# Performance work log

Measured on AMD Instinct MI355X. Metric: run time of the kernel, lower is better.

Reference implementation:

```python
import jax, jax.numpy as jnp
import numpy as np

HID = 1024
HEADS = 16
HEAD_DIM = HID // HEADS
MAX_P = 64
TAB = 2 * MAX_P + 1
B, L = 8, 512


def setup_inputs() -> dict:
    key = jax.random.key(0)
    ks = jax.random.split(key, 16)
    def lin(k, fan_in, fan_out):
        lim = 1.0 / np.sqrt(fan_in)
        kw, kb = jax.random.split(k)
        W = jax.random.uniform(kw, (fan_out, fan_in), jnp.float32, -lim, lim)
        b = jax.random.uniform(kb, (fan_out,), jnp.float32, -lim, lim)
        return W, b
    Wq, bq = lin(ks[0], HID, HID)
    Wk, bk = lin(ks[1], HID, HID)
    Wv, bv = lin(ks[2], HID, HID)
    Wo, bo = lin(ks[3], HID, HID)
    # xavier_uniform for relative-position tables
    xlim = float(np.sqrt(6.0 / (TAB + HEAD_DIM)))
    table_k = jax.random.uniform(ks[4], (TAB, HEAD_DIM), jnp.float32, -xlim, xlim)
    table_v = jax.random.uniform(ks[5], (TAB, HEAD_DIM), jnp.float32, -xlim, xlim)
    return {
        "query": jax.random.normal(ks[6], (B, L, HID), jnp.float32),
        "key": jax.random.normal(ks[7], (B, L, HID), jnp.float32),
        "value": jax.random.normal(ks[8], (B, L, HID), jnp.float32),
        "final_mat": jax.random.randint(ks[9], (B, L, L), 0, TAB, jnp.int64 if jax.config.jax_enable_x64 else jnp.int32),
        "Wq": Wq, "bq": bq, "Wk": Wk, "bk": bk,
        "Wv": Wv, "bv": bv, "Wo": Wo, "bo": bo,
        "table_k": table_k, "table_v": table_v,
    }


def reference(query, key, value, final_mat, Wq, bq, Wk, bk, Wv, bv, Wo, bo, table_k, table_v):
    Bt, Lq, D = query.shape
    H, hd = HEADS, HEAD_DIM
    q = query @ Wq.T + bq          # [B,Lq,D]
    k = key @ Wk.T + bk            # [B,Lk,D]
    v = value @ Wv.T + bv          # [B,Lv,D]
    q4 = q.reshape(Bt, Lq, H, hd)
    k4 = k.reshape(Bt, -1, H, hd)
    v4 = v.reshape(Bt, -1, H, hd)
    # content-content scores
    attn1 = jnp.einsum('bqhd,bkhd->bhqk', q4, k4)
    # content-position scores via gathered relative-key embeddings [B,Lq,Lk,hd]
    rk = table_k[final_mat]
    attn2 = jnp.einsum('bqhd,bqkd->bhqk', q4, rk)
    scale = jnp.asarray(np.sqrt(hd), q.dtype)
    attn = jax.nn.softmax((attn1 + attn2) / scale, axis=-1)  # [B,H,Lq,Lk]
    # dropout p=0 (eval)
    w1 = jnp.einsum('bhqk,bkhd->bqhd', attn, v4)
    rv = table_v[final_mat]                                   # [B,Lq,Lk,hd]
    w2 = jnp.einsum('bhqk,bqkd->bqhd', attn, rv)
    x = (w1 + w2).reshape(Bt, Lq, D)
    return x @ Wo.T + bo
```

## Files before the change

kernel.cpp:

```cpp
#include <hip/hip_runtime.h>

#define HID 1024
#define HEADS 16
#define HD 64
#define TAB 129
#define QSTR 136
#define BATCH 8
#define SEQ 512

typedef unsigned int uint;
typedef unsigned short ushort;
typedef unsigned char uchar;
typedef __attribute__((ext_vector_type(4))) float f32x4;
typedef __attribute__((ext_vector_type(8))) __bf16 bf16x8;

__device__ __forceinline__ ushort f2b(float x) {
    uint b = __float_as_uint(x);
    uint r = (b + 0x7fffu + ((b >> 16) & 1u)) >> 16;
    return (ushort)r;
}
__device__ __forceinline__ uint pk(float lo, float hi) {
    return (uint)f2b(lo) | ((uint)f2b(hi) << 16);
}
__device__ __forceinline__ float b2f(ushort u) {
    return __uint_as_float(((uint)u) << 16);
}
union U16x8 { uint u[4]; bf16x8 v; ushort s[8]; uint4 q; };
__device__ __forceinline__ bf16x8 pack8(float a0, float a1, float a2, float a3,
                                        float a4, float a5, float a6, float a7) {
    U16x8 r;
    r.u[0] = pk(a0, a1); r.u[1] = pk(a2, a3);
    r.u[2] = pk(a4, a5); r.u[3] = pk(a6, a7);
    return r.v;
}

#define GL16(gp, lp) __builtin_amdgcn_global_load_lds( \
    (const __attribute__((address_space(1))) void*)(gp), \
    (__attribute__((address_space(3))) void*)(lp), 16, 0, 0)

#define LDS_BARRIER() do { \
        asm volatile("s_waitcnt lgkmcnt(0)" ::: "memory"); \
        __builtin_amdgcn_s_barrier(); \
    } while (0)

struct ConvArgs { const float* src[7]; ushort* dst[7]; };

__global__ __launch_bounds__(256) void convert_bf16(ConvArgs ca) {
    int bid = blockIdx.x;
    int ti, lb;
    if (bid < 6144) { ti = bid >> 11; lb = bid & 2047; }
    else { int r = bid - 6144; ti = 3 + (r >> 9); lb = r & 511; }
    const float* s = ca.src[ti] + (size_t)lb * 2048 + (threadIdx.x << 3);
    ushort*      d = ca.dst[ti] + (size_t)lb * 2048 + (threadIdx.x << 3);
    float4 a = *(const float4*)s;
    float4 c = *(const float4*)(s + 4);
    uint4 u;
    u.x = pk(a.x, a.y); u.y = pk(a.z, a.w);
    u.z = pk(c.x, c.y); u.w = pk(c.z, c.w);
    *(uint4*)d = u;
}

struct GemmArgs {
    const ushort* A[3];
    const ushort* W[3];
    const float*  bias[3];
    ushort*       Cb[3];
};

__global__ __launch_bounds__(256) void gemm_qkv(GemmArgs ga) {
    const int N = HID, K = HID;
    __shared__ ushort As[2][128 * 32];
    __shared__ ushort Bs[2][128 * 32];
    const int tid = threadIdx.x;
    const int bid = blockIdx.x;
    const int swz = (bid & 7) * 96 + (bid >> 3);
    const int z   = swz >> 8;
    const int rem = swz & 255;
    const int m0  = (rem >> 3) * 128;
    const int n0  = (rem & 7) * 128;
    const ushort* A = ga.A[z];
    const ushort* W = ga.W[z];

    const int w  = tid >> 6;
    const int l  = tid & 63;
    const int lr = l & 15;
    const int lg = l >> 4;
    const int wm = w >> 1;
    const int wn = w & 1;

    const int sr = tid >> 2;
    const int sc = tid & 3;
    const int g  = sc ^ ((sr >> 1) & 3);
    const ushort* Ag0 = A + (size_t)(m0 + sr)      * K + g * 8;
    const ushort* Ag1 = A + (size_t)(m0 + sr + 64) * K + g * 8;
    const ushort* Wg0 = W + (size_t)(n0 + sr)      * K + g * 8;
    const ushort* Wg1 = W + (size_t)(n0 + sr + 64) * K + g * 8;

    f32x4 acc[4][4];
#pragma unroll
    for (int mt = 0; mt < 4; ++mt)
#pragma unroll
        for (int nt = 0; nt < 4; ++nt) acc[mt][nt] = (f32x4){0.f, 0.f, 0.f, 0.f};

#define STAGE(buf, k0) do { \
        GL16(Ag0 + (k0), &As[buf][w * 512]); \
        GL16(Ag1 + (k0), &As[buf][2048 + w * 512]); \
        GL16(Wg0 + (k0), &Bs[buf][w * 512]); \
        GL16(Wg1 + (k0), &Bs[buf][2048 + w * 512]); \
    } while (0)

    const int swl = (lr >> 1) & 3;
#define COMPUTE(buf) do { \
        bf16x8 af[4], bf[4]; \
        _Pragma("unroll") \
        for (int mt = 0; mt < 4; ++mt) \
            af[mt] = *(const bf16x8*)&As[buf][(wm * 64 + mt * 16 + lr) * 32 + (lg ^ swl) * 8]; \
        _Pragma("unroll") \
        for (int nt = 0; nt < 4; ++nt) \
            bf[nt] = *(const bf16x8*)&Bs[buf][(wn * 64 + nt * 16 + lr) * 32 + (lg ^ swl) * 8]; \
        _Pragma("unroll") \
        for (int mt = 0; mt < 4; ++mt) \
            _Pragma("unroll") \
            for (int nt = 0; nt < 4; ++nt) \
                acc[mt][nt] = __builtin_amdgcn_mfma_f32_16x16x32_bf16(af[mt], bf[nt], acc[mt][nt], 0, 0, 0); \
    } while (0)

    STAGE(0, 0);
    __syncthreads();
    const int nk = K / 32;
    for (int t = 0; t < nk - 1; ++t) {
        STAGE((t + 1) & 1, (size_t)(t + 1) * 32);
        COMPUTE(t & 1);
        __syncthreads();
    }
    COMPUTE((nk - 1) & 1);

    const float* bias = ga.bias[z];
    float bv[4];
#pragma unroll
    for (int nt = 0; nt < 4; ++nt) bv[nt] = bias[n0 + wn * 64 + nt * 16 + lr];
    ushort* Cb = ga.Cb[z];
#pragma unroll
    for (int mt = 0; mt < 4; ++mt)
#pragma unroll
        for (int r4 = 0; r4 < 4; ++r4) {
            size_t m = m0 + wm * 64 + mt * 16 + lg * 4 + r4;
            ushort* crow = Cb + m * N + n0 + wn * 64 + lr;
#pragma unroll
            for (int nt = 0; nt < 4; ++nt)
                crow[nt * 16] = f2b(acc[mt][nt][r4] + bv[nt]);
        }
#undef STAGE
#undef COMPUTE
}

__global__ __launch_bounds__(256) void gemm_wo(const ushort* __restrict__ A,
                                               const ushort* __restrict__ W,
                                               const float* __restrict__ bias,
                                               float* __restrict__ Cf) {
    const int N = HID, K = HID;
    __shared__ ushort As[2][128 * 32];
    __shared__ ushort Bs[2][64 * 32];
    const int tid = threadIdx.x;
    const int bid = blockIdx.x;
    const int swz = (bid & 7) * 64 + (bid >> 3);
    const int m0 = (swz >> 4) * 128;
    const int n0 = (swz & 15) * 64;

    const int w  = tid >> 6;
    const int l  = tid & 63;
    const int lr = l & 15;
    const int lg = l >> 4;
    const int wm = w >> 1;
    const int wn = w & 1;

    const int sr = tid >> 2;
    const int sc = tid & 3;
    const int g  = sc ^ ((sr >> 1) & 3);
    const ushort* Ag0 = A + (size_t)(m0 + sr)      * K + g * 8;
    const ushort* Ag1 = A + (size_t)(m0 + sr + 64) * K + g * 8;
    const ushort* Wg0 = W + (size_t)(n0 + sr)      * K + g * 8;

    f32x4 acc[4][2];
#pragma unroll
    for (int mt = 0; mt < 4; ++mt)
#pragma unroll
        for (int nt = 0; nt < 2; ++nt) acc[mt][nt] = (f32x4){0.f, 0.f, 0.f, 0.f};

#define STAGE(buf, k0) do { \
        GL16(Ag0 + (k0), &As[buf][w * 512]); \
        GL16(Ag1 + (k0), &As[buf][2048 + w * 512]); \
        GL16(Wg0 + (k0), &Bs[buf][w * 512]); \
    } while (0)

    const int swl = (lr >> 1) & 3;
#define COMPUTE(buf) do { \
        bf16x8 af[4], bf[2]; \
        _Pragma("unroll") \
        for (int mt = 0; mt < 4; ++mt) \
            af[mt] = *(const bf16x8*)&As[buf][(wm * 64 + mt * 16 + lr) * 32 + (lg ^ swl) * 8]; \
        _Pragma("unroll") \
        for (int nt = 0; nt < 2; ++nt) \
            bf[nt] = *(const bf16x8*)&Bs[buf][(wn * 32 + nt * 16 + lr) * 32 + (lg ^ swl) * 8]; \
        _Pragma("unroll") \
        for (int mt = 0; mt < 4; ++mt) \
            _Pragma("unroll") \
            for (int nt = 0; nt < 2; ++nt) \
                acc[mt][nt] = __builtin_amdgcn_mfma_f32_16x16x32_bf16(af[mt], bf[nt], acc[mt][nt], 0, 0, 0); \
    } while (0)

    STAGE(0, 0);
    __syncthreads();
    const int nk = K / 32;
    for (int t = 0; t < nk - 1; ++t) {
        STAGE((t + 1) & 1, (size_t)(t + 1) * 32);
        COMPUTE(t & 1);
        __syncthreads();
    }
    COMPUTE((nk - 1) & 1);

    float bv[2];
#pragma unroll
    for (int nt = 0; nt < 2; ++nt) bv[nt] = bias[n0 + wn * 32 + nt * 16 + lr];
#pragma unroll
    for (int mt = 0; mt < 4; ++mt)
#pragma unroll
        for (int r4 = 0; r4 < 4; ++r4) {
            size_t m = m0 + wm * 64 + mt * 16 + lg * 4 + r4;
            float* crow = Cf + m * N + n0 + wn * 32 + lr;
#pragma unroll
            for (int nt = 0; nt < 2; ++nt)
                crow[nt * 16] = acc[mt][nt][r4] + bv[nt];
        }
#undef STAGE
#undef COMPUTE
}

__global__ __launch_bounds__(256) void prep_kernel(const ushort* __restrict__ qb,
                                                   const float* __restrict__ table_k,
                                                   const ushort* __restrict__ vb,
                                                   const float* __restrict__ table_v,
                                                   const int* __restrict__ fmat,
                                                   ushort* __restrict__ qtab,
                                                   ushort* __restrict__ vT,
                                                   ushort* __restrict__ tvT2,
                                                   uchar* __restrict__ fm8) {
    __shared__ __align__(16) ushort shmem[144 * 72];
    const int wg  = blockIdx.x;
    const int tid = threadIdx.x;

    if (wg < 256) {
        const int h    = wg & 15;
        const int half = (wg >> 4) & 1;
        const int b    = wg >> 5;
        const int q0   = half * 256;
        ushort* tk = shmem;
        for (int i = tid; i < TAB * 8; i += 256) {
            int row = i >> 3, gr = i & 7;
            const float* src = table_k + row * HD + gr * 8;
            float4 a = *(const float4*)src;
            float4 c = *(const float4*)(src + 4);
            uint4 u;
            u.x = pk(a.x, a.y); u.y = pk(a.z, a.w);
            u.z = pk(c.x, c.y); u.w = pk(c.z, c.w);
            *(uint4*)&tk[row * 72 + gr * 8] = u;
        }
        __syncthreads();

        const int w  = tid >> 6;
        const int l  = tid & 63;
        const int lr = l & 15;
        const int lg = l >> 4;
        bf16x8 qf[4][2];
#pragma unroll
        for (int qt = 0; qt < 4; ++qt) {
            const ushort* qrow = qb + ((size_t)(b * SEQ) + q0 + w * 64 + qt * 16 + lr) * HID + h * HD;
            qf[qt][0] = *(const bf16x8*)(qrow + lg * 8);
            qf[qt][1] = *(const bf16x8*)(qrow + 32 + lg * 8);
        }
        ushort* outbase = qtab + ((size_t)(b * HEADS + h) * SEQ + q0 + w * 64) * QSTR;
#pragma unroll
        for (int mt = 0; mt < 9; ++mt) {
            bf16x8 tf0 = *(const bf16x8*)&tk[(mt * 16 + lr) * 72 + lg * 8];
            bf16x8 tf1 = *(const bf16x8*)&tk[(mt * 16 + lr) * 72 + 32 + lg * 8];
#pragma unroll
            for (int qt = 0; qt < 4; ++qt) {
                f32x4 acc = (f32x4){0.f, 0.f, 0.f, 0.f};
                acc = __builtin_amdgcn_mfma_f32_16x16x32_bf16(tf0, qf[qt][0], acc, 0, 0, 0);
                acc = __builtin_amdgcn_mfma_f32_16x16x32_bf16(tf1, qf[qt][1], acc, 0, 0, 0);
                ushort* orow = outbase + (size_t)(qt * 16 + lr) * QSTR;
                if (mt < 8) {
                    uint2 pu;
                    pu.x = pk(acc[0], acc[1]); pu.y = pk(acc[2], acc[3]);
                    *(uint2*)&orow[mt * 16 + lg * 4] = pu;
                } else if (lg == 0) {
                    orow[128] = f2b(acc[0]);
                }
            }
        }
    } else if (wg < 768) {
        const int vw = wg - 256;
        ushort* tile = shmem;
        const int b = vw >> 6, h = (vw >> 2) & 15, kc = vw & 3;
        const int k0 = kc * 128;
        {
            const int kr = tid >> 1, dc = (tid & 1) * 32;
            const ushort* src = vb + ((size_t)(b * SEQ) + k0 + kr) * HID + h * 64 + dc;
#pragma unroll
            for (int j = 0; j < 4; ++j) {
                uint4 u = *(const uint4*)(src + j * 8);
                *(uint4*)&tile[kr * 72 + dc + j * 8] = u;
            }
        }
        __syncthreads();
        {
            const int dr = tid >> 2, kc2 = (tid & 3) * 32;
            ushort* dst = vT + ((size_t)(b * 16 + h) * 64 + dr) * 512 + k0 + kc2;
#pragma unroll
            for (int j = 0; j < 4; ++j) {
                U16x8 o;
#pragma unroll
                for (int i = 0; i < 8; ++i)
                    o.s[i] = tile[(kc2 + j * 8 + i) * 72 + dr];
                *(uint4*)(dst + j * 8) = o.q;
            }
        }
    } else if (wg == 768) {
        for (int i = tid; i < 64 * 160; i += 256) {
            int d = i / 160;
            int c = i - d * 160;
            tvT2[i] = (c < TAB) ? f2b(table_v[(size_t)c * HD + d]) : (ushort)0;
        }
    } else {
        const size_t base = (size_t)(wg - 769) * 2048 + (size_t)tid * 8;
        int4 a = *(const int4*)(fmat + base);
        int4 c = *(const int4*)(fmat + base + 4);
        uint lo = (uint)a.x | ((uint)a.y << 8) | ((uint)a.z << 16) | ((uint)a.w << 24);
        uint hi = (uint)c.x | ((uint)c.y << 8) | ((uint)c.z << 16) | ((uint)c.w << 24);
        uint2 o; o.x = lo; o.y = hi;
        *(uint2*)(fm8 + base) = o;
    }
}

__global__ __launch_bounds__(256) void qk_gemm(const ushort* __restrict__ qb,
                                               const ushort* __restrict__ kb,
                                               ushort* __restrict__ S) {
    __shared__ ushort As[2][128 * 32];
    __shared__ ushort Bs[2][128 * 32];
    const int tid = threadIdx.x;
    const int m0 = blockIdx.x * 128;
    const int n0 = blockIdx.y * 128;
    const int bh = blockIdx.z;
    const int b = bh >> 4, h = bh & 15;
    const size_t rowQ = (size_t)b * SEQ;

    const int w  = tid >> 6;
    const int l  = tid & 63;
    const int lr = l & 15;
    const int lg = l >> 4;
    const int wm = w >> 1;
    const int wn = w & 1;

    const int sr = tid >> 2;
    const int sc = tid & 3;
    const int g  = sc ^ ((sr >> 1) & 3);
    const ushort* Ag0 = qb + (rowQ + m0 + sr)      * HID + h * HD + g * 8;
    const ushort* Ag1 = qb + (rowQ + m0 + sr + 64) * HID + h * HD + g * 8;
    const ushort* Wg0 = kb + (rowQ + n0 + sr)      * HID + h * HD + g * 8;
    const ushort* Wg1 = kb + (rowQ + n0 + sr + 64) * HID + h * HD + g * 8;

    GL16(Ag0,      &As[0][w * 512]); GL16(Ag1,      &As[0][2048 + w * 512]);
    GL16(Wg0,      &Bs[0][w * 512]); GL16(Wg1,      &Bs[0][2048 + w * 512]);
    GL16(Ag0 + 32, &As[1][w * 512]); GL16(Ag1 + 32, &As[1][2048 + w * 512]);
    GL16(Wg0 + 32, &Bs[1][w * 512]); GL16(Wg1 + 32, &Bs[1][2048 + w * 512]);

    f32x4 acc[4][4];
#pragma unroll
    for (int mt = 0; mt < 4; ++mt)
#pragma unroll
        for (int nt = 0; nt < 4; ++nt) acc[mt][nt] = (f32x4){0.f, 0.f, 0.f, 0.f};

    const int swl = (lr >> 1) & 3;
    __syncthreads();
#pragma unroll
    for (int buf = 0; buf < 2; ++buf) {
        bf16x8 af[4], bf[4];
#pragma unroll
        for (int mt = 0; mt < 4; ++mt)
            af[mt] = *(const bf16x8*)&As[buf][(wm * 64 + mt * 16 + lr) * 32 + (lg ^ swl) * 8];
#pragma unroll
        for (int nt = 0; nt < 4; ++nt)
            bf[nt] = *(const bf16x8*)&Bs[buf][(wn * 64 + nt * 16 + lr) * 32 + (lg ^ swl) * 8];
#pragma unroll
        for (int mt = 0; mt < 4; ++mt)
#pragma unroll
            for (int nt = 0; nt < 4; ++nt)
                acc[mt][nt] = __builtin_amdgcn_mfma_f32_16x16x32_bf16(af[mt], bf[nt], acc[mt][nt], 0, 0, 0);
    }

    ushort* Sb = S + (size_t)bh * SEQ * SEQ;
#pragma unroll
    for (int mt = 0; mt < 4; ++mt)
#pragma unroll
        for (int r4 = 0; r4 < 4; ++r4) {
            int m = m0 + wm * 64 + mt * 16 + lg * 4 + r4;
            ushort* srow = Sb + (size_t)m * SEQ + n0 + wn * 64 + lr;
#pragma unroll
            for (int nt = 0; nt < 4; ++nt)
                srow[nt * 16] = f2b(acc[mt][nt][r4]);
        }
}

__global__ __launch_bounds__(256) void smpv_kernel(const ushort* __restrict__ S,
                                                   const uchar* __restrict__ fm8,
                                                   const ushort* __restrict__ qt,
                                                   const ushort* __restrict__ vT,
                                                   const ushort* __restrict__ tvT2,
                                                   ushort* __restrict__ x) {
    constexpr float FIX = 65536.0f;
    constexpr float INV_FIX = 1.0f / 65536.0f;
    __shared__ __align__(16) uint   bins[64 * 132];
    __shared__ __align__(16) ushort qtb[64 * QSTR];
    __shared__ float rowsum[64];

    const int tid = threadIdx.x;
    const int w   = tid >> 6;
    const int l   = tid & 63;
    const int lr  = l & 15;
    const int lg  = l >> 4;

    const int bid = blockIdx.x;
    const int swz = (bid & 7) * 128 + (bid >> 3);
    const int bh  = swz >> 3;
    const int m0  = (swz & 7) * 64;
    const int b   = bh >> 4, h = bh & 15;

    {
        const uint4* src = (const uint4*)(qt + ((size_t)bh * SEQ + m0) * QSTR);
        uint4* dst = (uint4*)qtb;
        for (int i = tid; i < 64 * QSTR / 8; i += 256) dst[i] = src[i];
    }
    {
        uint4 z = {0u, 0u, 0u, 0u};
        uint4* dz = (uint4*)bins;
        for (int i = tid; i < 64 * 132 / 4; i += 256) dz[i] = z;
    }
    LDS_BARRIER();

    const int myrow = w * 16 + lr;
    const ushort* Srow  = S + ((size_t)bh * SEQ + m0 + myrow) * SEQ;
    const uchar*  fmrow = fm8 + ((size_t)(b * SEQ) + m0 + myrow) * SEQ;
    const ushort* qrow  = qtb + myrow * QSTR;
    uint*         brow  = bins + myrow * 132;
    const ushort* vbase = vT + (size_t)bh * 64 * 512;

    f32x4 acc[4];
#pragma unroll
    for (int nt = 0; nt < 4; ++nt) acc[nt] = (f32x4){0.f, 0.f, 0.f, 0.f};
    float lsum = 0.f;

    for (int ks = 0; ks < 16; ++ks) {
        const int k0 = ks * 32 + lg * 8;
        U16x8 sv;
        sv.q = *(const uint4*)(Srow + k0);
        uint2 fm = *(const uint2*)(fmrow + k0);
        int ts[8];
        ts[0] = fm.x & 255; ts[1] = (fm.x >> 8) & 255;
        ts[2] = (fm.x >> 16) & 255; ts[3] = fm.x >> 24;
        ts[4] = fm.y & 255; ts[5] = (fm.y >> 8) & 255;
        ts[6] = (fm.y >> 16) & 255; ts[7] = fm.y >> 24;
        float p[8];
#pragma unroll
        for (int j = 0; j < 8; ++j) {
            p[j] = __expf((b2f(sv.s[j]) + b2f(qrow[ts[j]])) * 0.125f);
            lsum += p[j];
        }
#pragma unroll
        for (int j = 0; j < 8; ++j)
            __hip_atomic_fetch_add(&brow[ts[j]], (uint)(p[j] * FIX),
                                   __ATOMIC_RELAXED, __HIP_MEMORY_SCOPE_WORKGROUP);
        bf16x8 af = pack8(p[0], p[1], p[2], p[3], p[4], p[5], p[6], p[7]);
#pragma unroll
        for (int nt = 0; nt < 4; ++nt) {
            bf16x8 bf_ = *(const bf16x8*)(vbase + (size_t)(nt * 16 + lr) * 512 + k0);
            acc[nt] = __builtin_amdgcn_mfma_f32_16x16x32_bf16(af, bf_, acc[nt], 0, 0, 0);
        }
    }
    lsum += __shfl_xor(lsum, 16);
    lsum += __shfl_xor(lsum, 32);
    if (lg == 0) rowsum[myrow] = lsum;

    asm volatile("s_waitcnt lgkmcnt(0)" ::: "memory");

#pragma unroll
    for (int ks = 0; ks < 4; ++ks) {
        const int t0 = ks * 32 + lg * 8;
        const uint* bp = brow + t0;
        bf16x8 af = pack8((float)bp[0] * INV_FIX, (float)bp[1] * INV_FIX,
                          (float)bp[2] * INV_FIX, (float)bp[3] * INV_FIX,
                          (float)bp[4] * INV_FIX, (float)bp[5] * INV_FIX,
                          (float)bp[6] * INV_FIX, (float)bp[7] * INV_FIX);
#pragma unroll
        for (int nt = 0; nt < 4; ++nt) {
            bf16x8 bf_ = *(const bf16x8*)(tvT2 + (size_t)(nt * 16 + lr) * 160 + t0);
            acc[nt] = __builtin_amdgcn_mfma_f32_16x16x32_bf16(af, bf_, acc[nt], 0, 0, 0);
        }
    }

    float iv[4], nb[4];
#pragma unroll
    for (int r = 0; r < 4; ++r) {
        const int crow = w * 16 + lg * 4 + r;
        iv[r] = 1.f / rowsum[crow];
        nb[r] = (float)bins[crow * 132 + 128] * INV_FIX;
    }
#pragma unroll
    for (int nt = 0; nt < 4; ++nt) {
        float tv = b2f(tvT2[(size_t)(nt * 16 + lr) * 160 + 128]);
#pragma unroll
        for (int r = 0; r < 4; ++r)
            acc[nt][r] = (acc[nt][r] + nb[r] * tv) * iv[r];
    }
    {
        ushort* orow = x + ((size_t)(b * SEQ) + m0 + w * 16 + lg * 4) * HID + h * HD;
#pragma unroll
        for (int r = 0; r < 4; ++r)
#pragma unroll
            for (int nt = 0; nt < 4; ++nt)
                orow[(size_t)r * HID + nt * 16 + lr] = f2b(acc[nt][r]);
    }
}

extern "C" void kernel_launch(void* const* d_in, const int* in_sizes, int n_in,
                              void* d_out, int out_size, void* d_ws, size_t ws_size,
                              hipStream_t stream) {
    const float* query = (const float*)d_in[0];
    const float* key   = (const float*)d_in[1];
    const float* value = (const float*)d_in[2];
    const int*   fmat  = (const int*)d_in[3];
    const float* Wq = (const float*)d_in[4];
    const float* bq = (const float*)d_in[5];
    const float* Wk = (const float*)d_in[6];
    const float* bk = (const float*)d_in[7];
    const float* Wv = (const float*)d_in[8];
    const float* bv = (const float*)d_in[9];
    const float* Wo = (const float*)d_in[10];
    const float* bo = (const float*)d_in[11];
    const float* table_k = (const float*)d_in[12];
    const float* table_v = (const float*)d_in[13];

    const size_t nBLD = (size_t)BATCH * SEQ * HID;
    const size_t nW   = (size_t)HID * HID;
    ushort* us = (ushort*)d_ws;
    ushort* qin16 = us;                 us += nBLD;
    ushort* kin16 = us;                 us += nBLD;
    ushort* vin16 = us;                 us += nBLD;
    ushort* wq16  = us;                 us += nW;
    ushort* wk16  = us;                 us += nW;
    ushort* wv16  = us;                 us += nW;
    ushort* wo16  = us;                 us += nW;
    ushort* qb16  = us;                 us += nBLD;
    ushort* kb16  = us;                 us += nBLD;
    ushort* vb16  = us;                 us += nBLD;
    ushort* qt16  = us;                 us += (size_t)BATCH * HEADS * SEQ * QSTR;
    ushort* xb16  = us;                 us += nBLD;
    uchar*  fm8   = (uchar*)us;         us += (size_t)BATCH * SEQ * SEQ / 2;
    ushort* Sbuf  = us;                 us += (size_t)BATCH * HEADS * SEQ * SEQ;

    ConvArgs ca;
    ca.src[0] = query; ca.src[1] = key; ca.src[2] = value;
    ca.src[3] = Wq; ca.src[4] = Wk; ca.src[5] = Wv; ca.src[6] = Wo;
    ca.dst[0] = qin16; ca.dst[1] = kin16; ca.dst[2] = vin16;
    ca.dst[3] = wq16; ca.dst[4] = wk16; ca.dst[5] = wv16; ca.dst[6] = wo16;
    convert_bf16<<<dim3(8192), 256, 0, stream>>>(ca);

    GemmArgs gq = {};
    gq.A[0] = qin16; gq.A[1] = kin16; gq.A[2] = vin16;
    gq.W[0] = wq16;  gq.W[1] = wk16;  gq.W[2] = wv16;
    gq.bias[0] = bq; gq.bias[1] = bk; gq.bias[2] = bv;
    gq.Cb[0] = qb16; gq.Cb[1] = kb16; gq.Cb[2] = vb16;
    gemm_qkv<<<dim3(768), 256, 0, stream>>>(gq);

    ushort* vTbuf  = qin16;
    ushort* tvTbuf = kin16;

    prep_kernel<<<dim3(1793), 256, 0, stream>>>(qb16, table_k, vb16, table_v,
                                                fmat, qt16, vTbuf, tvTbuf, fm8);

    qk_gemm<<<dim3(4, 4, 128), 256, 0, stream>>>(qb16, kb16, Sbuf);
    smpv_kernel<<<dim3(1024), 256, 0, stream>>>(Sbuf, fm8, qt16, vTbuf, tvTbuf, xb16);

    gemm_wo<<<dim3(512), 256, 0, stream>>>(xb16, wo16, bo, (float*)d_out);
}
```

Measured before the change: 179.4 us.

## Split smpv key dimension across two wave groups with LDS reduction

Doubles the smpv block to 512 threads and splits the 512-key loop into two halves, each handled by a group of four waves. The two groups share the atomic bins, and each takes half of the table_v bin chunks. Partial accumulators are then reduced through LDS, reusing the qt buffer, with row sums combined across the halves. This shortens the serial per-wave loop and adds latency-hiding waves, at the cost of extra barriers, an LDS reduction and more atomic contention on shared bins.

```diff
diff --git a/kernel.cpp b/kernel.cpp
--- a/kernel.cpp
+++ b/kernel.cpp
@@ -411,23 +411,25 @@
         }
 }
 
-__global__ __launch_bounds__(256) void smpv_kernel(const ushort* __restrict__ S,
-                                                   const uchar* __restrict__ fm8,
-                                                   const ushort* __restrict__ qt,
-                                                   const ushort* __restrict__ vT,
-                                                   const ushort* __restrict__ tvT2,
-                                                   ushort* __restrict__ x) {
+__global__ __launch_bounds__(512, 4) void smpv_kernel(const ushort* __restrict__ S,
+                                                      const uchar* __restrict__ fm8,
+                                                      const ushort* __restrict__ qt,
+                                                      const ushort* __restrict__ vT,
+                                                      const ushort* __restrict__ tvT2,
+                                                      ushort* __restrict__ x) {
     constexpr float FIX = 65536.0f;
     constexpr float INV_FIX = 1.0f / 65536.0f;
     __shared__ __align__(16) uint   bins[64 * 132];
     __shared__ __align__(16) ushort qtb[64 * QSTR];
-    __shared__ float rowsum[64];
+    __shared__ float rowsum[2][64];
 
     const int tid = threadIdx.x;
     const int w   = tid >> 6;
     const int l   = tid & 63;
     const int lr  = l & 15;
     const int lg  = l >> 4;
+    const int rg  = w & 3;
+    const int kh  = w >> 2;
 
     const int bid = blockIdx.x;
     const int swz = (bid & 7) * 128 + (bid >> 3);
@@ -438,28 +440,29 @@
     {
         const uint4* src = (const uint4*)(qt + ((size_t)bh * SEQ + m0) * QSTR);
         uint4* dst = (uint4*)qtb;
-        for (int i = tid; i < 64 * QSTR / 8; i += 256) dst[i] = src[i];
+        for (int i = tid; i < 64 * QSTR / 8; i += 512) dst[i] = src[i];
     }
     {
         uint4 z = {0u, 0u, 0u, 0u};
         uint4* dz = (uint4*)bins;
-        for (int i = tid; i < 64 * 132 / 4; i += 256) dz[i] = z;
+        for (int i = tid; i < 64 * 132 / 4; i += 512) dz[i] = z;
     }
     LDS_BARRIER();
 
-    const int myrow = w * 16 + lr;
-    const ushort* Srow  = S + ((size_t)bh * SEQ + m0 + myrow) * SEQ;
-    const uchar*  fmrow = fm8 + ((size_t)(b * SEQ) + m0 + myrow) * SEQ;
+    const int myrow = rg * 16 + lr;
+    const int kbase = kh * 256;
+    const ushort* Srow  = S + ((size_t)bh * SEQ + m0 + myrow) * SEQ + kbase;
+    const uchar*  fmrow = fm8 + ((size_t)(b * SEQ) + m0 + myrow) * SEQ + kbase;
     const ushort* qrow  = qtb + myrow * QSTR;
     uint*         brow  = bins + myrow * 132;
-    const ushort* vbase = vT + (size_t)bh * 64 * 512;
+    const ushort* vbase = vT + (size_t)bh * 64 * 512 + kbase;
 
     f32x4 acc[4];
 #pragma unroll
     for (int nt = 0; nt < 4; ++nt) acc[nt] = (f32x4){0.f, 0.f, 0.f, 0.f};
     float lsum = 0.f;
 
-    for (int ks = 0; ks < 16; ++ks) {
+    for (int ks = 0; ks < 8; ++ks) {
         const int k0 = ks * 32 + lg * 8;
         U16x8 sv;
         sv.q = *(const uint4*)(Srow + k0);
@@ -488,13 +491,13 @@
     }
     lsum += __shfl_xor(lsum, 16);
     lsum += __shfl_xor(lsum, 32);
-    if (lg == 0) rowsum[myrow] = lsum;
-
-    asm volatile("s_waitcnt lgkmcnt(0)" ::: "memory");
-
-#pragma unroll
-    for (int ks = 0; ks < 4; ++ks) {
-        const int t0 = ks * 32 + lg * 8;
+    if (lg == 0) rowsum[kh][myrow] = lsum;
+
+    LDS_BARRIER();
+
+#pragma unroll
+    for (int c = 0; c < 2; ++c) {
+        const int t0 = (kh * 2 + c) * 32 + lg * 8;
         const uint* bp = brow + t0;
         bf16x8 af = pack8((float)bp[0] * INV_FIX, (float)bp[1] * INV_FIX,
                           (float)bp[2] * INV_FIX, (float)bp[3] * INV_FIX,
@@ -507,22 +510,36 @@
         }
     }
 
-    float iv[4], nb[4];
-#pragma unroll
-    for (int r = 0; r < 4; ++r) {
-        const int crow = w * 16 + lg * 4 + r;
-        iv[r] = 1.f / rowsum[crow];
-        nb[r] = (float)bins[crow * 132 + 128] * INV_FIX;
-    }
-#pragma unroll
-    for (int nt = 0; nt < 4; ++nt) {
-        float tv = b2f(tvT2[(size_t)(nt * 16 + lr) * 160 + 128]);
-#pragma unroll
-        for (int r = 0; r < 4; ++r)
-            acc[nt][r] = (acc[nt][r] + nb[r] * tv) * iv[r];
-    }
-    {
-        ushort* orow = x + ((size_t)(b * SEQ) + m0 + w * 16 + lg * 4) * HID + h * HD;
+    float* obuf = (float*)qtb;
+    if (kh == 1) {
+#pragma unroll
+        for (int nt = 0; nt < 4; ++nt)
+            *(f32x4*)&obuf[((rg * 4 + nt) * 64 + l) * 4] = acc[nt];
+    }
+    LDS_BARRIER();
+
+    if (kh == 0) {
+#pragma unroll
+        for (int nt = 0; nt < 4; ++nt) {
+            f32x4 p_ = *(const f32x4*)&obuf[((rg * 4 + nt) * 64 + l) * 4];
+            acc[nt][0] += p_[0]; acc[nt][1] += p_[1];
+            acc[nt][2] += p_[2]; acc[nt][3] += p_[3];
+        }
+        float iv[4], nb[4];
+#pragma unroll
+        for (int r = 0; r < 4; ++r) {
+            const int crow = rg * 16 + lg * 4 + r;
+            iv[r] = 1.f / (rowsum[0][crow] + rowsum[1][crow]);
+            nb[r] = (float)bins[crow * 132 + 128] * INV_FIX;
+        }
+#pragma unroll
+        for (int nt = 0; nt < 4; ++nt) {
+            float tv = b2f(tvT2[(size_t)(nt * 16 + lr) * 160 + 128]);
+#pragma unroll
+            for (int r = 0; r < 4; ++r)
+                acc[nt][r] = (acc[nt][r] + nb[r] * tv) * iv[r];
+        }
+        ushort* orow = x + ((size_t)(b * SEQ) + m0 + rg * 16 + lg * 4) * HID + h * HD;
 #pragma unroll
         for (int r = 0; r < 4; ++r)
 #pragma unroll
@@ -588,7 +605,7 @@
                                                 fmat, qt16, vTbuf, tvTbuf, fm8);
 
     qk_gemm<<<dim3(4, 4, 128), 256, 0, stream>>>(qb16, kb16, Sbuf);
-    smpv_kernel<<<dim3(1024), 256, 0, stream>>>(Sbuf, fm8, qt16, vTbuf, tvTbuf, xb16);
+    smpv_kernel<<<dim3(1024), 512, 0, stream>>>(Sbuf, fm8, qt16, vTbuf, tvTbuf, xb16);
 
     gemm_wo<<<dim3(512), 256, 0, stream>>>(xb16, wo16, bo, (float*)d_out);
 }
```

Measured after the change: 167.7 us. 1.07x faster.
